# Kernel optimization log

Hardware: AMD Instinct MI355X
Metric: run time of the kernel (lower is better)

Reference implementation:

```python
import jax, jax.numpy as jnp
import numpy as np


def setup_inputs() -> dict:
    key = jax.random.key(0)
    k1, k2, k3 = jax.random.split(key, 3)
    B, L, D, H = 8, 1024, 768, 128
    text = jax.random.normal(k1, (B, L, D), dtype=jnp.float32)
    mask = jnp.ones((B, L), dtype=jnp.float32)  # accepted by forward but unused
    # nn.Linear-style init scale
    W0 = jax.random.normal(k2, (H, D), dtype=jnp.float32) / np.sqrt(D)
    b0 = jnp.zeros((H,), dtype=jnp.float32)
    W1 = jax.random.normal(k3, (1, 2 * H), dtype=jnp.float32) / np.sqrt(2 * H)
    b1 = jnp.zeros((1,), dtype=jnp.float32)
    return {"text": text, "mask": mask, "W0": W0, "b0": b0, "W1": W1, "b1": b1}


def reference(text, mask, W0, b0, W1, b1):
    # h = relu(linear0(text))  -> [B, L, 128]
    h = jax.nn.relu(jnp.einsum('bld,hd->blh', text, W0) + b0)
    H = W0.shape[0]
    # linear([h_i ; h_j]) = h_i @ w_a + h_j @ w_b + b  (split the 256->1 weight)
    w_a = W1[0, :H]   # weights applied to the row (i) copy
    w_b = W1[0, H:]   # weights applied to the column (j) copy
    s1 = jnp.einsum('blh,h->bl', h, w_a)  # [B, L]
    s2 = jnp.einsum('blh,h->bl', h, w_b)  # [B, L]
    # logits[b, i, j] = sigmoid(s1[b, i] + s2[b, j] + b1)
    logits = jax.nn.sigmoid(s1[:, :, None] + s2[:, None, :] + b1[0])
    return logits
```

## Files before the change

kernel.cpp:

```cpp
#include <hip/hip_runtime.h>

#define M_ROWS 8192
#define DIM    768
#define HCH    128

typedef __bf16 bf16x8 __attribute__((ext_vector_type(8)));
typedef float  f32x4  __attribute__((ext_vector_type(4)));

__device__ __forceinline__ unsigned short f2bf(float f) {
    union { float f; unsigned int u; } v; v.f = f;
    unsigned int u = v.u;
    u += 0x7fffu + ((u >> 16) & 1u);
    return (unsigned short)(u >> 16);
}

__global__ __launch_bounds__(256) void convert_w0_kernel(
    const float* __restrict__ W0, unsigned short* __restrict__ W0b)
{
    int i = (blockIdx.x * 256 + threadIdx.x) * 4;
    float4 v = *(const float4*)(W0 + i);
    uint2 o;
    o.x = (unsigned int)f2bf(v.x) | ((unsigned int)f2bf(v.y) << 16);
    o.y = (unsigned int)f2bf(v.z) | ((unsigned int)f2bf(v.w) << 16);
    *(uint2*)(W0b + i) = o;
}

__global__ __launch_bounds__(256) void gemm_s_kernel(
    const float* __restrict__ text,
    const unsigned short* __restrict__ W0b,
    const float* __restrict__ b0,
    const float* __restrict__ W1,
    float* __restrict__ s1, float* __restrict__ s2)
{
    __shared__ unsigned short As[32][40];
    __shared__ unsigned short Bs[128][40];
    __shared__ float red1[32][2];
    __shared__ float red2[32][2];

    const int tid  = threadIdx.x;
    const int lane = tid & 63;
    const int wave = tid >> 6;
    const int row0 = blockIdx.x * 32;

    const int wrow = (wave >> 1) * 16;
    const int wcol = (wave & 1) * 64;
    const int n16  = lane & 15;
    const int quad = lane >> 4;

    const int am  = tid >> 3;
    const int ak4 = (tid & 7) << 2;
    const int bn  = tid >> 2;
    const int bp  = tid & 3;

    const float*          aptr  = text + (size_t)(row0 + am) * DIM + ak4;
    const unsigned short* bptr0 = W0b + (size_t)bn * DIM + bp * 8;
    const unsigned short* bptr1 = bptr0 + (size_t)64 * DIM;

    f32x4 acc[4];
    #pragma unroll
    for (int j = 0; j < 4; ++j) acc[j] = (f32x4){0.f, 0.f, 0.f, 0.f};

    float4 av  = *(const float4*)aptr;
    uint4  bv0 = *(const uint4*)bptr0;
    uint4  bv1 = *(const uint4*)bptr1;

    for (int kt = 0; kt < DIM; kt += 32) {
        const int ktn = (kt + 32 < DIM) ? (kt + 32) : 0;
        float4 av_n  = *(const float4*)(aptr + ktn);
        uint4  bv0_n = *(const uint4*)(bptr0 + ktn);
        uint4  bv1_n = *(const uint4*)(bptr1 + ktn);

        uint2 o;
        o.x = (unsigned int)f2bf(av.x) | ((unsigned int)f2bf(av.y) << 16);
        o.y = (unsigned int)f2bf(av.z) | ((unsigned int)f2bf(av.w) << 16);
        *(uint2*)&As[am][ak4]         = o;
        *(uint4*)&Bs[bn][bp * 8]      = bv0;
        *(uint4*)&Bs[bn + 64][bp * 8] = bv1;
        __syncthreads();

        bf16x8 a   = *(const bf16x8*)&As[wrow + n16][quad * 8];
        bf16x8 bf0 = *(const bf16x8*)&Bs[wcol +  0 + n16][quad * 8];
        bf16x8 bf1 = *(const bf16x8*)&Bs[wcol + 16 + n16][quad * 8];
        bf16x8 bf2 = *(const bf16x8*)&Bs[wcol + 32 + n16][quad * 8];
        bf16x8 bf3 = *(const bf16x8*)&Bs[wcol + 48 + n16][quad * 8];
        acc[0] = __builtin_amdgcn_mfma_f32_16x16x32_bf16(a, bf0, acc[0], 0, 0, 0);
        acc[1] = __builtin_amdgcn_mfma_f32_16x16x32_bf16(a, bf1, acc[1], 0, 0, 0);
        acc[2] = __builtin_amdgcn_mfma_f32_16x16x32_bf16(a, bf2, acc[2], 0, 0, 0);
        acc[3] = __builtin_amdgcn_mfma_f32_16x16x32_bf16(a, bf3, acc[3], 0, 0, 0);
        __syncthreads();

        av = av_n; bv0 = bv0_n; bv1 = bv1_n;
    }

    float p1[4] = {0.f, 0.f, 0.f, 0.f};
    float p2[4] = {0.f, 0.f, 0.f, 0.f};
    #pragma unroll
    for (int j = 0; j < 4; ++j) {
        const int col = wcol + j * 16 + n16;
        const float bb = b0[col];
        const float wa = W1[col];
        const float wb = W1[HCH + col];
        #pragma unroll
        for (int r = 0; r < 4; ++r) {
            float h = acc[j][r] + bb;
            h = fmaxf(h, 0.f);
            p1[r] += h * wa;
            p2[r] += h * wb;
        }
    }
    #pragma unroll
    for (int r = 0; r < 4; ++r) {
        #pragma unroll
        for (int m = 8; m >= 1; m >>= 1) {
            p1[r] += __shfl_xor(p1[r], m);
            p2[r] += __shfl_xor(p2[r], m);
        }
    }
    if (n16 == 0) {
        #pragma unroll
        for (int r = 0; r < 4; ++r) {
            const int rr = wrow + quad * 4 + r;
            red1[rr][wave & 1] = p1[r];
            red2[rr][wave & 1] = p2[r];
        }
    }
    __syncthreads();
    if (tid < 32) {
        s1[row0 + tid] = red1[tid][0] + red1[tid][1];
        s2[row0 + tid] = red2[tid][0] + red2[tid][1];
    }
}

__global__ __launch_bounds__(256) void outer_sigmoid_kernel(
    const float* __restrict__ s1, const float* __restrict__ s2,
    const float* __restrict__ b1, float* __restrict__ out)
{
    const int bi = blockIdx.x;
    const int b  = bi >> 10;
    const float base = s1[bi] + b1[0];
    const float4 t = ((const float4*)(s2 + (b << 10)))[threadIdx.x];
    float4 r;
    r.x = 1.f / (1.f + __expf(-(base + t.x)));
    r.y = 1.f / (1.f + __expf(-(base + t.y)));
    r.z = 1.f / (1.f + __expf(-(base + t.z)));
    r.w = 1.f / (1.f + __expf(-(base + t.w)));
    ((float4*)out)[((size_t)bi << 8) + threadIdx.x] = r;
}

extern "C" void kernel_launch(void* const* d_in, const int* in_sizes, int n_in,
                              void* d_out, int out_size, void* d_ws, size_t ws_size,
                              hipStream_t stream)
{
    const float* text = (const float*)d_in[0];
    const float* W0 = (const float*)d_in[2];
    const float* b0 = (const float*)d_in[3];
    const float* W1 = (const float*)d_in[4];
    const float* b1 = (const float*)d_in[5];
    float* out = (float*)d_out;

    unsigned short* W0b = (unsigned short*)d_ws;
    float* s1 = (float*)((char*)d_ws + (size_t)HCH * DIM * sizeof(unsigned short));
    float* s2 = s1 + M_ROWS;

    convert_w0_kernel<<<96, 256, 0, stream>>>(W0, W0b);
    gemm_s_kernel<<<256, 256, 0, stream>>>(text, W0b, b0, W1, s1, s2);
    outer_sigmoid_kernel<<<8192, 256, 0, stream>>>(s1, s2, b1, out);
}
```

Baseline: 96.71 us.

## Fuse W0 bf16 conversion into GEMM and halve row tile to 16

Drops the separate W0-to-bf16 conversion kernel; the GEMM now loads fp32 W0 directly and converts it while staging into shared memory. The row tile shrinks from 32 to 16, so the grid doubles to 512 blocks. The four waves now split the 128 output columns instead of a 2x2 row/column split, and the final reduction sums four partials per row. This removes one kernel launch and raises block count for occupancy, at the cost of each block re-reading and re-converting the full fp32 W0, which doubles weight traffic and conversion work per row.

Result: slower. 104.1 us (+7.7%).

```diff
diff --git a/kernel.cpp b/kernel.cpp
--- a/kernel.cpp
+++ b/kernel.cpp
@@ -13,89 +13,90 @@
     u += 0x7fffu + ((u >> 16) & 1u);
     return (unsigned short)(u >> 16);
 }
-
-__global__ __launch_bounds__(256) void convert_w0_kernel(
-    const float* __restrict__ W0, unsigned short* __restrict__ W0b)
-{
-    int i = (blockIdx.x * 256 + threadIdx.x) * 4;
-    float4 v = *(const float4*)(W0 + i);
-    uint2 o;
-    o.x = (unsigned int)f2bf(v.x) | ((unsigned int)f2bf(v.y) << 16);
-    o.y = (unsigned int)f2bf(v.z) | ((unsigned int)f2bf(v.w) << 16);
-    *(uint2*)(W0b + i) = o;
+__device__ __forceinline__ unsigned int pk2bf(float x, float y) {
+    return (unsigned int)f2bf(x) | ((unsigned int)f2bf(y) << 16);
 }
 
 __global__ __launch_bounds__(256) void gemm_s_kernel(
     const float* __restrict__ text,
-    const unsigned short* __restrict__ W0b,
+    const float* __restrict__ W0,
     const float* __restrict__ b0,
     const float* __restrict__ W1,
     float* __restrict__ s1, float* __restrict__ s2)
 {
-    __shared__ unsigned short As[32][40];
+    __shared__ unsigned short As[16][40];
     __shared__ unsigned short Bs[128][40];
-    __shared__ float red1[32][2];
-    __shared__ float red2[32][2];
+    __shared__ float red1[16][4];
+    __shared__ float red2[16][4];
 
     const int tid  = threadIdx.x;
     const int lane = tid & 63;
     const int wave = tid >> 6;
-    const int row0 = blockIdx.x * 32;
+    const int row0 = blockIdx.x * 16;
 
-    const int wrow = (wave >> 1) * 16;
-    const int wcol = (wave & 1) * 64;
     const int n16  = lane & 15;
     const int quad = lane >> 4;
+    const int wcol = wave * 32;
 
-    const int am  = tid >> 3;
-    const int ak4 = (tid & 7) << 2;
-    const int bn  = tid >> 2;
-    const int bp  = tid & 3;
+    const int ar = tid >> 3;
+    const int ak = (tid & 7) << 2;
+    const int br = tid >> 1;
+    const int bk = (tid & 1) << 4;
 
-    const float*          aptr  = text + (size_t)(row0 + am) * DIM + ak4;
-    const unsigned short* bptr0 = W0b + (size_t)bn * DIM + bp * 8;
-    const unsigned short* bptr1 = bptr0 + (size_t)64 * DIM;
+    const float* aptr = text + (size_t)(row0 + ar) * DIM + ak;
+    const float* bptr = W0 + (size_t)br * DIM + bk;
 
-    f32x4 acc[4];
+    f32x4 acc[2];
+    acc[0] = (f32x4){0.f, 0.f, 0.f, 0.f};
+    acc[1] = (f32x4){0.f, 0.f, 0.f, 0.f};
+
+    float4 av, bv[4];
+    if (tid < 128) av = *(const float4*)aptr;
     #pragma unroll
-    for (int j = 0; j < 4; ++j) acc[j] = (f32x4){0.f, 0.f, 0.f, 0.f};
-
-    float4 av  = *(const float4*)aptr;
-    uint4  bv0 = *(const uint4*)bptr0;
-    uint4  bv1 = *(const uint4*)bptr1;
+    for (int q = 0; q < 4; ++q) bv[q] = *(const float4*)(bptr + q * 4);
 
     for (int kt = 0; kt < DIM; kt += 32) {
         const int ktn = (kt + 32 < DIM) ? (kt + 32) : 0;
-        float4 av_n  = *(const float4*)(aptr + ktn);
-        uint4  bv0_n = *(const uint4*)(bptr0 + ktn);
-        uint4  bv1_n = *(const uint4*)(bptr1 + ktn);
+        float4 av_n, bv_n[4];
+        if (tid < 128) av_n = *(const float4*)(aptr + ktn);
+        #pragma unroll
+        for (int q = 0; q < 4; ++q) bv_n[q] = *(const float4*)(bptr + ktn + q * 4);
 
-        uint2 o;
-        o.x = (unsigned int)f2bf(av.x) | ((unsigned int)f2bf(av.y) << 16);
-        o.y = (unsigned int)f2bf(av.z) | ((unsigned int)f2bf(av.w) << 16);
-        *(uint2*)&As[am][ak4]         = o;
-        *(uint4*)&Bs[bn][bp * 8]      = bv0;
-        *(uint4*)&Bs[bn + 64][bp * 8] = bv1;
+        if (tid < 128) {
+            uint2 o;
+            o.x = pk2bf(av.x, av.y);
+            o.y = pk2bf(av.z, av.w);
+            *(uint2*)&As[ar][ak] = o;
+        }
+        uint4 ob;
+        ob.x = pk2bf(bv[0].x, bv[0].y);
+        ob.y = pk2bf(bv[0].z, bv[0].w);
+        ob.z = pk2bf(bv[1].x, bv[1].y);
+        ob.w = pk2bf(bv[1].z, bv[1].w);
+        *(uint4*)&Bs[br][bk] = ob;
+        ob.x = pk2bf(bv[2].x, bv[2].y);
+        ob.y = pk2bf(bv[2].z, bv[2].w);
+        ob.z = pk2bf(bv[3].x, bv[3].y);
+        ob.w = pk2bf(bv[3].z, bv[3].w);
+        *(uint4*)&Bs[br][bk + 8] = ob;
         __syncthreads();
 
-        bf16x8 a   = *(const bf16x8*)&As[wrow + n16][quad * 8];
+        bf16x8 a   = *(const bf16x8*)&As[n16][quad * 8];
         bf16x8 bf0 = *(const bf16x8*)&Bs[wcol +  0 + n16][quad * 8];
         bf16x8 bf1 = *(const bf16x8*)&Bs[wcol + 16 + n16][quad * 8];
-        bf16x8 bf2 = *(const bf16x8*)&Bs[wcol + 32 + n16][quad * 8];
-        bf16x8 bf3 = *(const bf16x8*)&Bs[wcol + 48 + n16][quad * 8];
         acc[0] = __builtin_amdgcn_mfma_f32_16x16x32_bf16(a, bf0, acc[0], 0, 0, 0);
         acc[1] = __builtin_amdgcn_mfma_f32_16x16x32_bf16(a, bf1, acc[1], 0, 0, 0);
-        acc[2] = __builtin_amdgcn_mfma_f32_16x16x32_bf16(a, bf2, acc[2], 0, 0, 0);
-        acc[3] = __builtin_amdgcn_mfma_f32_16x16x32_bf16(a, bf3, acc[3], 0, 0, 0);
         __syncthreads();
 
-        av = av_n; bv0 = bv0_n; bv1 = bv1_n;
+        av = av_n;
+        #pragma unroll
+        for (int q = 0; q < 4; ++q) bv[q] = bv_n[q];
     }
 
     float p1[4] = {0.f, 0.f, 0.f, 0.f};
     float p2[4] = {0.f, 0.f, 0.f, 0.f};
     #pragma unroll
-    for (int j = 0; j < 4; ++j) {
+    for (int j = 0; j < 2; ++j) {
         const int col = wcol + j * 16 + n16;
         const float bb = b0[col];
         const float wa = W1[col];
@@ -119,15 +120,15 @@
     if (n16 == 0) {
         #pragma unroll
         for (int r = 0; r < 4; ++r) {
-            const int rr = wrow + quad * 4 + r;
-            red1[rr][wave & 1] = p1[r];
-            red2[rr][wave & 1] = p2[r];
+            const int rr = quad * 4 + r;
+            red1[rr][wave] = p1[r];
+            red2[rr][wave] = p2[r];
         }
     }
     __syncthreads();
-    if (tid < 32) {
-        s1[row0 + tid] = red1[tid][0] + red1[tid][1];
-        s2[row0 + tid] = red2[tid][0] + red2[tid][1];
+    if (tid < 16) {
+        s1[row0 + tid] = red1[tid][0] + red1[tid][1] + red1[tid][2] + red1[tid][3];
+        s2[row0 + tid] = red2[tid][0] + red2[tid][1] + red2[tid][2] + red2[tid][3];
     }
 }
 
@@ -158,11 +159,9 @@
     const float* b1 = (const float*)d_in[5];
     float* out = (float*)d_out;
 
-    unsigned short* W0b = (unsigned short*)d_ws;
-    float* s1 = (float*)((char*)d_ws + (size_t)HCH * DIM * sizeof(unsigned short));
+    float* s1 = (float*)d_ws;
     float* s2 = s1 + M_ROWS;
 
-    convert_w0_kernel<<<96, 256, 0, stream>>>(W0, W0b);
-    gemm_s_kernel<<<256, 256, 0, stream>>>(text, W0b, b0, W1, s1, s2);
+    gemm_s_kernel<<<512, 256, 0, stream>>>(text, W0, b0, W1, s1, s2);
     outer_sigmoid_kernel<<<8192, 256, 0, stream>>>(s1, s2, b1, out);
 }
```
